# Performance work log

Measured on AMD Instinct MI355X. Metric: run time of the kernel, lower is better.

## Reference

```python
import jax, jax.numpy as jnp
import numpy as np

B, S, E, H, DK, DV, DF = 4, 2048, 512, 8, 64, 64, 2048
EPS = 1e-3  # keras LayerNormalization default epsilon


def setup_inputs() -> dict:
    key = jax.random.key(0)
    ks = jax.random.split(key, 24)
    def n(k, shape, scale=0.02):
        return jax.random.normal(k, shape, jnp.float32) * scale
    inp = {}
    inp["x"] = jax.random.normal(ks[0], (B, S, E), jnp.float32)
    inp["encoder_output"] = jax.random.normal(ks[1], (B, S, E), jnp.float32)
    # lookahead mask: 1 above the diagonal (masked), broadcast over batch/heads
    inp["lookahead_mask"] = jnp.triu(jnp.ones((S, S), jnp.int32), k=1)[None, None]
    # padding mask: 0 = keep (no padding in this synthetic batch)
    inp["padding_mask"] = jnp.zeros((B, 1, 1, S), jnp.int32)
    # self-attention params
    inp["sa_Wq"] = n(ks[2], (E, H * DK)); inp["sa_bq"] = jnp.zeros((H * DK,), jnp.float32)
    inp["sa_Wk"] = n(ks[3], (E, H * DK)); inp["sa_bk"] = jnp.zeros((H * DK,), jnp.float32)
    inp["sa_Wv"] = n(ks[4], (E, H * DV)); inp["sa_bv"] = jnp.zeros((H * DV,), jnp.float32)
    inp["sa_Wo"] = n(ks[5], (H * DV, E)); inp["sa_bo"] = jnp.zeros((E,), jnp.float32)
    # cross-attention params
    inp["ca_Wq"] = n(ks[6], (E, H * DK)); inp["ca_bq"] = jnp.zeros((H * DK,), jnp.float32)
    inp["ca_Wk"] = n(ks[7], (E, H * DK)); inp["ca_bk"] = jnp.zeros((H * DK,), jnp.float32)
    inp["ca_Wv"] = n(ks[8], (E, H * DV)); inp["ca_bv"] = jnp.zeros((H * DV,), jnp.float32)
    inp["ca_Wo"] = n(ks[9], (H * DV, E)); inp["ca_bo"] = jnp.zeros((E,), jnp.float32)
    # feed-forward params
    inp["ff_W1"] = n(ks[10], (E, DF)); inp["ff_b1"] = jnp.zeros((DF,), jnp.float32)
    inp["ff_W2"] = n(ks[11], (DF, E)); inp["ff_b2"] = jnp.zeros((E,), jnp.float32)
    # layernorm params (3 add&norm blocks)
    for i in (1, 2, 3):
        inp[f"ln{i}_g"] = jnp.ones((E,), jnp.float32)
        inp[f"ln{i}_b"] = jnp.zeros((E,), jnp.float32)
    return inp


def _mha(q_in, k_in, v_in, mask, Wq, bq, Wk, bk, Wv, bv, Wo, bo):
    Bq, Sq, _ = q_in.shape
    Sk = k_in.shape[1]
    q = (q_in @ Wq + bq).reshape(Bq, Sq, H, DK).transpose(0, 2, 1, 3)  # bhqd
    k = (k_in @ Wk + bk).reshape(Bq, Sk, H, DK).transpose(0, 2, 1, 3)  # bhkd
    v = (v_in @ Wv + bv).reshape(Bq, Sk, H, DV).transpose(0, 2, 1, 3)  # bhkd
    scores = jnp.einsum("bhqd,bhkd->bhqk", q, k) / jnp.sqrt(jnp.float32(DK))
    scores = scores - 1e9 * mask.astype(scores.dtype)  # additive mask (1 = masked)
    attn = jax.nn.softmax(scores, axis=-1)
    out = jnp.einsum("bhqk,bhkd->bhqd", attn, v)
    out = out.transpose(0, 2, 1, 3).reshape(Bq, Sq, H * DV)
    return out @ Wo + bo


def _add_norm(x, sub, g, b):
    y = x + sub
    m = jnp.mean(y, axis=-1, keepdims=True)
    v = jnp.var(y, axis=-1, keepdims=True)
    return (y - m) / jnp.sqrt(v + EPS) * g + b


def reference(x, encoder_output, lookahead_mask, padding_mask,
              sa_Wq, sa_bq, sa_Wk, sa_bk, sa_Wv, sa_bv, sa_Wo, sa_bo,
              ca_Wq, ca_bq, ca_Wk, ca_bk, ca_Wv, ca_bv, ca_Wo, ca_bo,
              ff_W1, ff_b1, ff_W2, ff_b2,
              ln1_g, ln1_b, ln2_g, ln2_b, ln3_g, ln3_b):
    # dropout is identity at inference (training=False)
    a1 = _mha(x, x, x, lookahead_mask,
              sa_Wq, sa_bq, sa_Wk, sa_bk, sa_Wv, sa_bv, sa_Wo, sa_bo)
    x1 = _add_norm(x, a1, ln1_g, ln1_b)
    a2 = _mha(x1, encoder_output, encoder_output, padding_mask,
              ca_Wq, ca_bq, ca_Wk, ca_bk, ca_Wv, ca_bv, ca_Wo, ca_bo)
    x2 = _add_norm(x1, a2, ln2_g, ln2_b)
    ff = jax.nn.relu(x2 @ ff_W1 + ff_b1) @ ff_W2 + ff_b2
    return _add_norm(x2, ff, ln3_g, ln3_b)
```

## Files before the change

kernel.cpp:

```cpp
#include <hip/hip_runtime.h>

#define Bx  4
#define Sx  2048
#define Ex  512
#define Hx  8
#define Tt  (Bx * Sx)

typedef short          short8 __attribute__((ext_vector_type(8)));
typedef float          f32x4  __attribute__((ext_vector_type(4)));
typedef unsigned short u16;

__device__ __forceinline__ u16 f2bf(float f) {
    unsigned int u = __float_as_uint(f);
    u += 0x7fffu + ((u >> 16) & 1u);
    return (u16)(u >> 16);
}
__device__ __forceinline__ float bf2f(u16 h) {
    return __uint_as_float(((unsigned int)h) << 16);
}

__global__ __launch_bounds__(256) void f32_to_bf16_2(const float* __restrict__ a,
                                                     const float* __restrict__ b,
                                                     u16* __restrict__ oa,
                                                     u16* __restrict__ ob)
{
    const float* in  = blockIdx.y ? b : a;
    u16*         out = blockIdx.y ? ob : oa;
    int i = (blockIdx.x * 256 + threadIdx.x) << 2;
    float4 v = *(const float4*)(in + i);
    ushort4 o;
    o.x = f2bf(v.x); o.y = f2bf(v.y); o.z = f2bf(v.z); o.w = f2bf(v.w);
    *(ushort4*)(out + i) = o;
}

__global__ __launch_bounds__(256) void transpose_bf16(const float* __restrict__ W,
                                                      u16* __restrict__ Wt,
                                                      int K, int N)
{
    __shared__ u16 tile[32][33];
    const int n0 = blockIdx.x * 32, k0 = blockIdx.y * 32;
    const int tx = threadIdx.x & 31, ty = threadIdx.x >> 5;
#pragma unroll
    for (int i = 0; i < 32; i += 8)
        tile[ty + i][tx] = f2bf(W[(size_t)(k0 + ty + i) * N + n0 + tx]);
    __syncthreads();
#pragma unroll
    for (int i = 0; i < 32; i += 8)
        Wt[(size_t)(n0 + ty + i) * K + k0 + tx] = tile[tx][ty + i];
}

struct WPtrs { const float* w[8]; };
__global__ __launch_bounds__(256) void transpose8_bf16(WPtrs ws, u16* __restrict__ base)
{
    __shared__ u16 tile[32][33];
    const float* W  = ws.w[blockIdx.z];
    u16*         Wt = base + (size_t)blockIdx.z * 262144;
    const int n0 = blockIdx.x * 32, k0 = blockIdx.y * 32;
    const int tx = threadIdx.x & 31, ty = threadIdx.x >> 5;
#pragma unroll
    for (int i = 0; i < 32; i += 8)
        tile[ty + i][tx] = f2bf(W[(size_t)(k0 + ty + i) * 512 + n0 + tx]);
    __syncthreads();
#pragma unroll
    for (int i = 0; i < 32; i += 8)
        Wt[(size_t)(n0 + ty + i) * 512 + k0 + tx] = tile[tx][ty + i];
}

template<int OUT_BF16, int RELU>
__global__ __launch_bounds__(256) void gemm128(const u16* __restrict__ A,
                                               const u16* __restrict__ Bt,
                                               const float* __restrict__ b0,
                                               const float* __restrict__ b1,
                                               const float* __restrict__ b2,
                                               const float* __restrict__ b3,
                                               void* __restrict__ Cout,
                                               int M, int N, int K, int ldc)
{
    __shared__ u16 As[128 * 40];
    __shared__ u16 Bs[128 * 40];

    const int tid  = threadIdx.x;
    const int w    = tid >> 6;
    const int lane = tid & 63;
    const int c    = lane & 15;
    const int quad = lane >> 4;
    const int wr   = w >> 1, wc = w & 1;
    const int m0   = blockIdx.y * 128;
    const int n0   = blockIdx.x * 128;

    const int row0 = tid >> 2;
    const int kc   = (tid & 3) << 3;

    const u16* Ap = A  + (size_t)(m0 + row0) * K + kc;
    const u16* Bp = Bt + (size_t)(n0 + row0) * K + kc;
    const size_t rstep = (size_t)64 * K;

    f32x4 acc[4][4];
#pragma unroll
    for (int i = 0; i < 4; i++)
#pragma unroll
        for (int j = 0; j < 4; j++) { acc[i][j][0]=0.f; acc[i][j][1]=0.f; acc[i][j][2]=0.f; acc[i][j][3]=0.f; }

    short8 ra0 = *(const short8*)(Ap);
    short8 ra1 = *(const short8*)(Ap + rstep);
    short8 rb0 = *(const short8*)(Bp);
    short8 rb1 = *(const short8*)(Bp + rstep);

    for (int k0 = 0; k0 < K; k0 += 32) {
        __syncthreads();
        *(short8*)&As[row0 * 40 + kc]        = ra0;
        *(short8*)&As[(row0 + 64) * 40 + kc] = ra1;
        *(short8*)&Bs[row0 * 40 + kc]        = rb0;
        *(short8*)&Bs[(row0 + 64) * 40 + kc] = rb1;
        __syncthreads();

        if (k0 + 32 < K) {
            ra0 = *(const short8*)(Ap + k0 + 32);
            ra1 = *(const short8*)(Ap + rstep + k0 + 32);
            rb0 = *(const short8*)(Bp + k0 + 32);
            rb1 = *(const short8*)(Bp + rstep + k0 + 32);
        }

        short8 af[4], bf[4];
#pragma unroll
        for (int i = 0; i < 4; i++)
            af[i] = *(const short8*)&As[(wr * 64 + i * 16 + c) * 40 + quad * 8];
#pragma unroll
        for (int j = 0; j < 4; j++)
            bf[j] = *(const short8*)&Bs[(wc * 64 + j * 16 + c) * 40 + quad * 8];
#pragma unroll
        for (int i = 0; i < 4; i++)
#pragma unroll
            for (int j = 0; j < 4; j++)
                acc[i][j] = __builtin_amdgcn_mfma_f32_16x16x32_bf16(af[i], bf[j], acc[i][j], 0, 0, 0);
    }

    const int seg = n0 >> 9;
    const float* bp = seg == 0 ? b0 : (seg == 1 ? b1 : (seg == 2 ? b2 : b3));
    const int nbase = n0 & 511;
    float bv[4];
#pragma unroll
    for (int j = 0; j < 4; j++) bv[j] = bp[nbase + wc * 64 + j * 16 + c];

#pragma unroll
    for (int i = 0; i < 4; i++) {
#pragma unroll
        for (int j = 0; j < 4; j++) {
            int colg = n0 + wc * 64 + j * 16 + c;
#pragma unroll
            for (int r = 0; r < 4; r++) {
                int rowg = m0 + wr * 64 + i * 16 + quad * 4 + r;
                float v = acc[i][j][r] + bv[j];
                if (RELU) v = fmaxf(v, 0.f);
                if (OUT_BF16) ((u16*)Cout)[(size_t)rowg * ldc + colg] = f2bf(v);
                else          ((float*)Cout)[(size_t)rowg * ldc + colg] = v;
            }
        }
    }
}

template<int OUT_BF16, int RELU>
__global__ __launch_bounds__(128) void gemm64(const u16* __restrict__ A,
                                              const u16* __restrict__ Bt,
                                              const float* __restrict__ bias,
                                              void* __restrict__ Cout,
                                              int M, int N, int K, int ldc)
{
    __shared__ u16 As[128 * 40];
    __shared__ u16 Bs[64 * 40];

    const int tid  = threadIdx.x;
    const int w    = tid >> 6;
    const int lane = tid & 63;
    const int c    = lane & 15;
    const int quad = lane >> 4;
    const int m0   = blockIdx.y * 128;
    const int n0   = blockIdx.x * 64;

    const int rA = tid >> 2;
    const int kc = (tid & 3) << 3;

    const u16* Ap = A  + (size_t)(m0 + rA) * K + kc;
    const u16* Bp = Bt + (size_t)(n0 + rA) * K + kc;
    const size_t a32 = (size_t)32 * K;

    f32x4 acc[4][4];
#pragma unroll
    for (int i = 0; i < 4; i++)
#pragma unroll
        for (int j = 0; j < 4; j++) { acc[i][j][0]=0.f; acc[i][j][1]=0.f; acc[i][j][2]=0.f; acc[i][j][3]=0.f; }

    short8 ra[4], rb[2];
#pragma unroll
    for (int i = 0; i < 4; i++) ra[i] = *(const short8*)(Ap + i * a32);
#pragma unroll
    for (int i = 0; i < 2; i++) rb[i] = *(const short8*)(Bp + i * a32);

    for (int k0 = 0; k0 < K; k0 += 32) {
        __syncthreads();
#pragma unroll
        for (int i = 0; i < 4; i++) *(short8*)&As[(rA + i * 32) * 40 + kc] = ra[i];
#pragma unroll
        for (int i = 0; i < 2; i++) *(short8*)&Bs[(rA + i * 32) * 40 + kc] = rb[i];
        __syncthreads();

        if (k0 + 32 < K) {
#pragma unroll
            for (int i = 0; i < 4; i++) ra[i] = *(const short8*)(Ap + i * a32 + k0 + 32);
#pragma unroll
            for (int i = 0; i < 2; i++) rb[i] = *(const short8*)(Bp + i * a32 + k0 + 32);
        }

        short8 af[4], bf[4];
#pragma unroll
        for (int i = 0; i < 4; i++)
            af[i] = *(const short8*)&As[(w * 64 + i * 16 + c) * 40 + quad * 8];
#pragma unroll
        for (int j = 0; j < 4; j++)
            bf[j] = *(const short8*)&Bs[(j * 16 + c) * 40 + quad * 8];
#pragma unroll
        for (int i = 0; i < 4; i++)
#pragma unroll
            for (int j = 0; j < 4; j++)
                acc[i][j] = __builtin_amdgcn_mfma_f32_16x16x32_bf16(af[i], bf[j], acc[i][j], 0, 0, 0);
    }

    float bv[4];
#pragma unroll
    for (int j = 0; j < 4; j++) bv[j] = bias[n0 + j * 16 + c];

#pragma unroll
    for (int i = 0; i < 4; i++) {
#pragma unroll
        for (int j = 0; j < 4; j++) {
            int colg = n0 + j * 16 + c;
#pragma unroll
            for (int r = 0; r < 4; r++) {
                int rowg = m0 + w * 64 + i * 16 + quad * 4 + r;
                float v = acc[i][j][r] + bv[j];
                if (RELU) v = fmaxf(v, 0.f);
                if (OUT_BF16) ((u16*)Cout)[(size_t)rowg * ldc + colg] = f2bf(v);
                else          ((float*)Cout)[(size_t)rowg * ldc + colg] = v;
            }
        }
    }
}

template<bool CAUSAL>
__global__ __launch_bounds__(256) void attn_mfma(const u16* __restrict__ Q,
                                                 const u16* __restrict__ K,
                                                 const u16* __restrict__ V,
                                                 u16* __restrict__ O,
                                                 int ldq, int ldk, int ldv)
{
    __shared__ u16          Klds[32 * 72];
    __shared__ u16          Vtlds[64 * 40];
    __shared__ unsigned int Plds[4][16 * 18];

    const int tid  = threadIdx.x;
    const int w    = tid >> 6;
    const int lane = tid & 63;
    const int c    = lane & 15;
    const int quad = lane >> 4;
    const int q0   = blockIdx.x * 64;
    const int bh   = blockIdx.y;
    const int b    = bh >> 3;
    const int h    = bh & 7;
    const int bS   = b * Sx;
    const int hoff = h * 64;
    const int qw   = q0 + w * 16;

    const int kkey = tid >> 3;
    const int kc8  = (tid & 7) << 3;
    const int vdim = tid & 63;
    const int vp   = (tid >> 6) << 3;

    short8 qa[2];
    {
        const u16* qp = Q + (size_t)(bS + qw + c) * ldq + hoff;
        qa[0] = *(const short8*)(qp + quad * 8);
        qa[1] = *(const short8*)(qp + 32 + quad * 8);
    }

    f32x4 of[4];
#pragma unroll
    for (int f = 0; f < 4; f++) { of[f][0]=0.f; of[f][1]=0.f; of[f][2]=0.f; of[f][3]=0.f; }
    float lpart[4] = {0.f, 0.f, 0.f, 0.f};

    const int kend = CAUSAL ? (q0 + 64) : Sx;
    for (int kt = 0; kt < kend; kt += 32) {
        __syncthreads();
        *(short8*)&Klds[kkey * 72 + kc8] =
            *(const short8*)(K + (size_t)(bS + kt + kkey) * ldk + hoff + kc8);
        {
            const u16* gv = V + (size_t)(bS + kt) * ldv + hoff + vdim;
            union { short8 v; u16 u[8]; } vb;
#pragma unroll
            for (int j = 0; j < 8; j++) {
                int pos = vp + j;
                int key = (pos >> 1) + ((pos & 1) << 4);
                vb.u[j] = gv[(size_t)key * ldv];
            }
            *(short8*)&Vtlds[vdim * 40 + vp] = vb.v;
        }
        __syncthreads();

        int fmax = 2;
        if (CAUSAL) {
            int d = ((qw + 15 - kt) >> 4) + 1;
            fmax = d < 2 ? d : 2;
        }

        if (fmax > 0) {
            f32x4 s[2];
#pragma unroll
            for (int f = 0; f < 2; f++) {
                if (f < fmax) {
                    short8 kb0 = *(const short8*)&Klds[(f * 16 + c) * 72 + quad * 8];
                    short8 kb1 = *(const short8*)&Klds[(f * 16 + c) * 72 + 32 + quad * 8];
                    f32x4 z; z[0]=0.f; z[1]=0.f; z[2]=0.f; z[3]=0.f;
                    z = __builtin_amdgcn_mfma_f32_16x16x32_bf16(qa[0], kb0, z, 0, 0, 0);
                    z = __builtin_amdgcn_mfma_f32_16x16x32_bf16(qa[1], kb1, z, 0, 0, 0);
                    s[f] = z;
                }
            }

#pragma unroll
            for (int r = 0; r < 4; r++) {
                int qg = qw + quad * 4 + r;
                float p0 = 0.f, p1 = 0.f;
                if (!(CAUSAL && (kt + c) > qg))
                    p0 = __expf(s[0][r] * 0.125f);
                if (fmax > 1 && !(CAUSAL && (kt + 16 + c) > qg))
                    p1 = __expf(s[1][r] * 0.125f);
                u16 b0 = f2bf(p0), b1 = f2bf(p1);
                lpart[r] += bf2f(b0) + bf2f(b1);
                *(volatile unsigned int*)&Plds[w][(quad * 4 + r) * 18 + c] =
                    (unsigned int)b0 | ((unsigned int)b1 << 16);
            }

            union { unsigned int u[4]; short8 s8; } pu;
#pragma unroll
            for (int i = 0; i < 4; i++)
                pu.u[i] = *(volatile const unsigned int*)&Plds[w][c * 18 + quad * 4 + i];
            short8 pa = pu.s8;

#pragma unroll
            for (int f2 = 0; f2 < 4; f2++) {
                short8 vbf = *(const short8*)&Vtlds[(f2 * 16 + c) * 40 + quad * 8];
                of[f2] = __builtin_amdgcn_mfma_f32_16x16x32_bf16(pa, vbf, of[f2], 0, 0, 0);
            }
        }
    }

#pragma unroll
    for (int r = 0; r < 4; r++) {
        float v = lpart[r];
        v += __shfl_xor(v, 1, 64);
        v += __shfl_xor(v, 2, 64);
        v += __shfl_xor(v, 4, 64);
        v += __shfl_xor(v, 8, 64);
        lpart[r] = 1.f / v;
    }

    u16* Ob = O + (size_t)(bS + qw) * Ex + hoff;
#pragma unroll
    for (int f = 0; f < 4; f++)
#pragma unroll
        for (int r = 0; r < 4; r++)
            Ob[(size_t)(quad * 4 + r) * Ex + f * 16 + c] = f2bf(of[f][r] * lpart[r]);
}

__global__ __launch_bounds__(256) void ln_add(const float* __restrict__ x,
                                              const float* __restrict__ s,
                                              const float* __restrict__ g,
                                              const float* __restrict__ bta,
                                              float* __restrict__ out,
                                              u16* __restrict__ out_bf)
{
    __shared__ float red[8];
    const int    row  = blockIdx.x;
    const int    t    = threadIdx.x;
    const size_t base = (size_t)row * Ex;

    float2 xv = *(const float2*)(x + base + (t << 1));
    float2 sv = *(const float2*)(s + base + (t << 1));
    float  y0 = xv.x + sv.x;
    float  y1 = xv.y + sv.y;

    float sum = y0 + y1;
    float sq  = y0 * y0 + y1 * y1;
#pragma unroll
    for (int o = 32; o > 0; o >>= 1) {
        sum += __shfl_down(sum, o, 64);
        sq  += __shfl_down(sq,  o, 64);
    }
    const int wid = t >> 6, lane = t & 63;
    if (lane == 0) { red[wid] = sum; red[4 + wid] = sq; }
    __syncthreads();
    if (t == 0) {
        red[0] = red[0] + red[1] + red[2] + red[3];
        red[4] = red[4] + red[5] + red[6] + red[7];
    }
    __syncthreads();

    const float mean = red[0] * (1.f / 512.f);
    const float var  = red[4] * (1.f / 512.f) - mean * mean;
    const float rstd = rsqrtf(var + 1e-3f);

    float2 gv = *(const float2*)(g   + (t << 1));
    float2 bv = *(const float2*)(bta + (t << 1));
    float  o0 = (y0 - mean) * rstd * gv.x + bv.x;
    float  o1 = (y1 - mean) * rstd * gv.y + bv.y;
    *(float2*)(out + base + (t << 1)) = make_float2(o0, o1);
    if (out_bf) {
        ushort2 ob; ob.x = f2bf(o0); ob.y = f2bf(o1);
        *(ushort2*)(out_bf + base + (t << 1)) = ob;
    }
}

extern "C" void kernel_launch(void* const* d_in, const int* in_sizes, int n_in,
                              void* d_out, int out_size, void* d_ws, size_t ws_size,
                              hipStream_t stream)
{
    const float* x     = (const float*)d_in[0];
    const float* enc   = (const float*)d_in[1];
    const float* sa_Wq = (const float*)d_in[4],  *sa_bq = (const float*)d_in[5];
    const float* sa_Wk = (const float*)d_in[6],  *sa_bk = (const float*)d_in[7];
    const float* sa_Wv = (const float*)d_in[8],  *sa_bv = (const float*)d_in[9];
    const float* sa_Wo = (const float*)d_in[10], *sa_bo = (const float*)d_in[11];
    const float* ca_Wq = (const float*)d_in[12], *ca_bq = (const float*)d_in[13];
    const float* ca_Wk = (const float*)d_in[14], *ca_bk = (const float*)d_in[15];
    const float* ca_Wv = (const float*)d_in[16], *ca_bv = (const float*)d_in[17];
    const float* ca_Wo = (const float*)d_in[18], *ca_bo = (const float*)d_in[19];
    const float* ff_W1 = (const float*)d_in[20], *ff_b1 = (const float*)d_in[21];
    const float* ff_W2 = (const float*)d_in[22], *ff_b2 = (const float*)d_in[23];
    const float* ln1_g = (const float*)d_in[24], *ln1_b = (const float*)d_in[25];
    const float* ln2_g = (const float*)d_in[26], *ln2_b = (const float*)d_in[27];
    const float* ln3_g = (const float*)d_in[28], *ln3_b = (const float*)d_in[29];

    char* ws = (char*)d_ws;
    const size_t MB = 1024 * 1024;
    u16*   bw   = (u16*)(ws);
    u16*   xb   = (u16*)(ws + 8  * MB);
    u16*   encb = (u16*)(ws + 16 * MB);
    u16*   qkvB = (u16*)(ws + 24 * MB);
    u16*   qb   = (u16*)(ws + 24 * MB);
    u16*   kvB  = (u16*)(ws + 32 * MB);
    u16*   ff1b = (u16*)(ws + 24 * MB);
    u16*   ob   = (u16*)(ws + 48 * MB);
    float* projF= (float*)(ws + 56 * MB);
    float* x1f  = (float*)(ws + 72 * MB);
    u16*   x1b  = (u16*)(ws + 88 * MB);
    u16*   x2b  = (u16*)(ws + 88 * MB);
    float* x2f  = (float*)(ws + 8  * MB);

    u16* wsaq = bw;
    u16* wsao = bw + 786432;
    u16* wcaq = bw + 1048576;
    u16* wcak = bw + 1310720;
    u16* wcao = bw + 1835008;
    u16* wff1 = bw + 2097152;
    u16* wff2 = bw + 3145728;

    f32_to_bf16_2<<<dim3(Tt * Ex / 1024, 2), dim3(256), 0, stream>>>(x, enc, xb, encb);
    WPtrs wp; wp.w[0]=sa_Wq; wp.w[1]=sa_Wk; wp.w[2]=sa_Wv; wp.w[3]=sa_Wo;
    wp.w[4]=ca_Wq; wp.w[5]=ca_Wk; wp.w[6]=ca_Wv; wp.w[7]=ca_Wo;
    transpose8_bf16<<<dim3(16, 16, 8), dim3(256), 0, stream>>>(wp, bw);
    transpose_bf16<<<dim3(64, 16), dim3(256), 0, stream>>>(ff_W1, wff1, 512, 2048);
    transpose_bf16<<<dim3(16, 64), dim3(256), 0, stream>>>(ff_W2, wff2, 2048, 512);

    auto G128 = [&](const u16* A, const u16* Wt, const float* b0, const float* b1,
                    const float* b2, const float* b3, void* C,
                    int N, int K, int ldc, int out_bf, int relu) {
        dim3 grid(N / 128, Tt / 128);
        if (out_bf) {
            if (relu) gemm128<1,1><<<grid, dim3(256), 0, stream>>>(A, Wt, b0,b1,b2,b3, C, Tt, N, K, ldc);
            else      gemm128<1,0><<<grid, dim3(256), 0, stream>>>(A, Wt, b0,b1,b2,b3, C, Tt, N, K, ldc);
        } else        gemm128<0,0><<<grid, dim3(256), 0, stream>>>(A, Wt, b0,b1,b2,b3, C, Tt, N, K, ldc);
    };
    auto G64 = [&](const u16* A, const u16* Wt, const float* bi, void* C,
                   int K, int ldc, int out_bf) {
        dim3 grid(512 / 64, Tt / 128);
        if (out_bf) gemm64<1,0><<<grid, dim3(128), 0, stream>>>(A, Wt, bi, C, Tt, 512, K, ldc);
        else        gemm64<0,0><<<grid, dim3(128), 0, stream>>>(A, Wt, bi, C, Tt, 512, K, ldc);
    };
    const dim3 agrid(Sx / 64, Bx * Hx);

    G128(xb, wsaq, sa_bq, sa_bk, sa_bv, sa_bv, qkvB, 1536, 512, 1536, 1, 0);
    attn_mfma<true><<<agrid, dim3(256), 0, stream>>>(qkvB, qkvB + 512, qkvB + 1024,
                                                     ob, 1536, 1536, 1536);
    G64(ob, wsao, sa_bo, projF, 512, 512, 0);
    ln_add<<<dim3(Tt), dim3(256), 0, stream>>>(x, projF, ln1_g, ln1_b, x1f, x1b);

    G64(x1b, wcaq, ca_bq, qb, 512, 512, 1);
    G128(encb, wcak, ca_bk, ca_bv, ca_bv, ca_bv, kvB, 1024, 512, 1024, 1, 0);
    attn_mfma<false><<<agrid, dim3(256), 0, stream>>>(qb, kvB, kvB + 512,
                                                      ob, 512, 1024, 1024);
    G64(ob, wcao, ca_bo, projF, 512, 512, 0);
    ln_add<<<dim3(Tt), dim3(256), 0, stream>>>(x1f, projF, ln2_g, ln2_b, x2f, x2b);

    G128(x2b, wff1, ff_b1, ff_b1 + 512, ff_b1 + 1024, ff_b1 + 1536,
         ff1b, 2048, 512, 2048, 1, 1);
    G64(ff1b, wff2, ff_b2, projF, 2048, 512, 0);
    ln_add<<<dim3(Tt), dim3(256), 0, stream>>>(x2f, projF, ln3_g, ln3_b,
                                               (float*)d_out, (u16*)nullptr);
}
```

Baseline: 525.1 us.

## Double key tile to 64, prefetch K/V into registers, remap attention blocks

The attention kernel now processes 64 keys per iteration instead of 32, halving the number of barrier-separated iterations. K and V tiles are prefetched into registers one iteration ahead so global loads overlap the MFMA and softmax work. V is loaded with vectorized row reads and transposed into LDS with scalar stores, replacing eight strided scalar global loads. The block index is remapped to interleave heads and batches across blocks, which may balance the causal load. This costs more LDS and registers, and may waste masked work on the diagonal tile.

```diff
diff --git a/kernel.cpp b/kernel.cpp
--- a/kernel.cpp
+++ b/kernel.cpp
@@ -253,27 +253,30 @@
                                                  u16* __restrict__ O,
                                                  int ldq, int ldk, int ldv)
 {
-    __shared__ u16          Klds[32 * 72];
-    __shared__ u16          Vtlds[64 * 40];
-    __shared__ unsigned int Plds[4][16 * 18];
+    __shared__ u16          Klds[64 * 76];
+    __shared__ u16          Vtlds[64 * 74];
+    __shared__ unsigned int Plds[4][16 * 34];
 
     const int tid  = threadIdx.x;
     const int w    = tid >> 6;
     const int lane = tid & 63;
     const int c    = lane & 15;
     const int quad = lane >> 4;
-    const int q0   = blockIdx.x * 64;
-    const int bh   = blockIdx.y;
+
+    const int flat = blockIdx.y * 32 + blockIdx.x;
+    const int idx  = flat >> 3;
+    const int bh   = (flat & 7) * 4 + (idx >> 5);
+    const int q0   = (idx & 31) * 64;
+
     const int b    = bh >> 3;
     const int h    = bh & 7;
     const int bS   = b * Sx;
     const int hoff = h * 64;
     const int qw   = q0 + w * 16;
 
-    const int kkey = tid >> 3;
-    const int kc8  = (tid & 7) << 3;
-    const int vdim = tid & 63;
-    const int vp   = (tid >> 6) << 3;
+    const int skey = tid >> 3;
+    const int sd0  = (tid & 7) << 3;
+    const int vp0  = ((skey & 15) << 1) + (skey >> 4);
 
     short8 qa[2];
     {
@@ -288,67 +291,90 @@
     float lpart[4] = {0.f, 0.f, 0.f, 0.f};
 
     const int kend = CAUSAL ? (q0 + 64) : Sx;
-    for (int kt = 0; kt < kend; kt += 32) {
+
+    const u16* Kg = K + (size_t)(bS + skey) * ldk + hoff + sd0;
+    const u16* Vg = V + (size_t)(bS + skey) * ldv + hoff + sd0;
+    const size_t k32 = (size_t)32 * ldk;
+    const size_t v32 = (size_t)32 * ldv;
+    short8 kr0 = *(const short8*)(Kg);
+    short8 kr1 = *(const short8*)(Kg + k32);
+    short8 vr0 = *(const short8*)(Vg);
+    short8 vr1 = *(const short8*)(Vg + v32);
+
+    for (int kt = 0; kt < kend; kt += 64) {
         __syncthreads();
-        *(short8*)&Klds[kkey * 72 + kc8] =
-            *(const short8*)(K + (size_t)(bS + kt + kkey) * ldk + hoff + kc8);
-        {
-            const u16* gv = V + (size_t)(bS + kt) * ldv + hoff + vdim;
-            union { short8 v; u16 u[8]; } vb;
-#pragma unroll
-            for (int j = 0; j < 8; j++) {
-                int pos = vp + j;
-                int key = (pos >> 1) + ((pos & 1) << 4);
-                vb.u[j] = gv[(size_t)key * ldv];
-            }
-            *(short8*)&Vtlds[vdim * 40 + vp] = vb.v;
+        *(short8*)&Klds[skey * 76 + sd0]        = kr0;
+        *(short8*)&Klds[(skey + 32) * 76 + sd0] = kr1;
+#pragma unroll
+        for (int j = 0; j < 8; j++) {
+            Vtlds[(sd0 + j) * 74 + vp0]      = (u16)vr0[j];
+            Vtlds[(sd0 + j) * 74 + 32 + vp0] = (u16)vr1[j];
         }
         __syncthreads();
 
-        int fmax = 2;
+        if (kt + 64 < kend) {
+            Kg += (size_t)64 * ldk;  Vg += (size_t)64 * ldv;
+            kr0 = *(const short8*)(Kg);
+            kr1 = *(const short8*)(Kg + k32);
+            vr0 = *(const short8*)(Vg);
+            vr1 = *(const short8*)(Vg + v32);
+        }
+
+        int fmax = 4;
         if (CAUSAL) {
             int d = ((qw + 15 - kt) >> 4) + 1;
-            fmax = d < 2 ? d : 2;
-        }
-
-        if (fmax > 0) {
-            f32x4 s[2];
-#pragma unroll
-            for (int f = 0; f < 2; f++) {
-                if (f < fmax) {
-                    short8 kb0 = *(const short8*)&Klds[(f * 16 + c) * 72 + quad * 8];
-                    short8 kb1 = *(const short8*)&Klds[(f * 16 + c) * 72 + 32 + quad * 8];
-                    f32x4 z; z[0]=0.f; z[1]=0.f; z[2]=0.f; z[3]=0.f;
-                    z = __builtin_amdgcn_mfma_f32_16x16x32_bf16(qa[0], kb0, z, 0, 0, 0);
-                    z = __builtin_amdgcn_mfma_f32_16x16x32_bf16(qa[1], kb1, z, 0, 0, 0);
-                    s[f] = z;
-                }
+            fmax = d < 4 ? d : 4;
+        }
+        const bool hi = !CAUSAL || fmax > 2;
+
+        f32x4 s[4];
+#pragma unroll
+        for (int f = 0; f < 4; f++) {
+            if (f < fmax) {
+                short8 kb0 = *(const short8*)&Klds[(f * 16 + c) * 76 + quad * 8];
+                short8 kb1 = *(const short8*)&Klds[(f * 16 + c) * 76 + 32 + quad * 8];
+                f32x4 z; z[0]=0.f; z[1]=0.f; z[2]=0.f; z[3]=0.f;
+                z = __builtin_amdgcn_mfma_f32_16x16x32_bf16(qa[0], kb0, z, 0, 0, 0);
+                z = __builtin_amdgcn_mfma_f32_16x16x32_bf16(qa[1], kb1, z, 0, 0, 0);
+                s[f] = z;
             }
-
-#pragma unroll
-            for (int r = 0; r < 4; r++) {
-                int qg = qw + quad * 4 + r;
-                float p0 = 0.f, p1 = 0.f;
-                if (!(CAUSAL && (kt + c) > qg))
-                    p0 = __expf(s[0][r] * 0.125f);
-                if (fmax > 1 && !(CAUSAL && (kt + 16 + c) > qg))
-                    p1 = __expf(s[1][r] * 0.125f);
-                u16 b0 = f2bf(p0), b1 = f2bf(p1);
-                lpart[r] += bf2f(b0) + bf2f(b1);
-                *(volatile unsigned int*)&Plds[w][(quad * 4 + r) * 18 + c] =
-                    (unsigned int)b0 | ((unsigned int)b1 << 16);
-            }
-
-            union { unsigned int u[4]; short8 s8; } pu;
+        }
+
+#pragma unroll
+        for (int r = 0; r < 4; r++) {
+            int qg = qw + quad * 4 + r;
+            float p0 = 0.f, p1 = 0.f, p2 = 0.f, p3 = 0.f;
+            if (0 < fmax && !(CAUSAL && (kt +  0 + c) > qg)) p0 = __expf(s[0][r] * 0.125f);
+            if (1 < fmax && !(CAUSAL && (kt + 16 + c) > qg)) p1 = __expf(s[1][r] * 0.125f);
+            if (2 < fmax && !(CAUSAL && (kt + 32 + c) > qg)) p2 = __expf(s[2][r] * 0.125f);
+            if (3 < fmax && !(CAUSAL && (kt + 48 + c) > qg)) p3 = __expf(s[3][r] * 0.125f);
+            u16 b0 = f2bf(p0), b1 = f2bf(p1), b2 = f2bf(p2), b3 = f2bf(p3);
+            lpart[r] += (bf2f(b0) + bf2f(b1)) + (bf2f(b2) + bf2f(b3));
+            volatile unsigned int* pr = &Plds[w][(quad * 4 + r) * 34];
+            pr[c] = (unsigned int)b0 | ((unsigned int)b1 << 16);
+            if (hi) pr[16 + c] = (unsigned int)b2 | ((unsigned int)b3 << 16);
+        }
+
+        union { unsigned int u[4]; short8 s8; } pa0, pa1;
+#pragma unroll
+        for (int i = 0; i < 4; i++)
+            pa0.u[i] = *(volatile const unsigned int*)&Plds[w][c * 34 + quad * 4 + i];
+        if (hi) {
 #pragma unroll
             for (int i = 0; i < 4; i++)
-                pu.u[i] = *(volatile const unsigned int*)&Plds[w][c * 18 + quad * 4 + i];
-            short8 pa = pu.s8;
-
+                pa1.u[i] = *(volatile const unsigned int*)&Plds[w][c * 34 + 16 + quad * 4 + i];
+        }
+
+#pragma unroll
+        for (int f2 = 0; f2 < 4; f2++) {
+            short8 vb0 = *(const short8*)&Vtlds[(f2 * 16 + c) * 74 + quad * 8];
+            of[f2] = __builtin_amdgcn_mfma_f32_16x16x32_bf16(pa0.s8, vb0, of[f2], 0, 0, 0);
+        }
+        if (hi) {
 #pragma unroll
             for (int f2 = 0; f2 < 4; f2++) {
-                short8 vbf = *(const short8*)&Vtlds[(f2 * 16 + c) * 40 + quad * 8];
-                of[f2] = __builtin_amdgcn_mfma_f32_16x16x32_bf16(pa, vbf, of[f2], 0, 0, 0);
+                short8 vb1 = *(const short8*)&Vtlds[(f2 * 16 + c) * 74 + 32 + quad * 8];
+                of[f2] = __builtin_amdgcn_mfma_f32_16x16x32_bf16(pa1.s8, vb1, of[f2], 0, 0, 0);
             }
         }
     }
```

New measurement: 576.1 us. 1.1x slower.
